# Kernel tuning notes

Hardware: AMD Instinct MI355X
Metric: run time of the kernel (lower is better)

## Reference

```python
import jax, jax.numpy as jnp
import numpy as np
from jax import lax


def _layernorm(x, scale, bias, eps=1e-5):
    m = x.mean(-1, keepdims=True)
    v = x.var(-1, keepdims=True)
    return (x - m) / jnp.sqrt(v + eps) * scale + bias


def setup_inputs() -> dict:
    key = jax.random.key(0)
    d = 21                      # code distance
    S = d * d - 1               # 440 tokens
    g = d + 1                   # 22x22 grid
    D, H, F, L, B = 256, 8, 512, 6, 64
    ks = jax.random.split(key, 24)
    w = 0.02
    idx = np.arange(S)
    scatter_positions = jnp.asarray(np.stack([idx // g, idx % g], axis=1), dtype=jnp.int64)
    inp = {
        'x': jax.random.randint(ks[0], (B, S), 0, 2).astype(jnp.int64),
        'scatter_positions': scatter_positions,
        'event_emb': w * jax.random.normal(ks[1], (2, D), jnp.float32),
        'pos_x': w * jax.random.normal(ks[2], (2 * d + 1, D), jnp.float32),
        'pos_y': w * jax.random.normal(ks[3], (2 * d + 1, D), jnp.float32),
        'stab_emb': w * jax.random.normal(ks[4], (2, D), jnp.float32),
        'tok_x': jax.random.randint(ks[5], (S,), 0, 2 * d + 1).astype(jnp.int64),
        'tok_y': jax.random.randint(ks[6], (S,), 0, 2 * d + 1).astype(jnp.int64),
        'tok_stab': jax.random.randint(ks[7], (S,), 0, 2).astype(jnp.int64),
        'attn_bias': w * jax.random.normal(ks[8], (S, S), jnp.float32),
        'Wqkv': w * jax.random.normal(ks[9], (L, 3 * D, D), jnp.float32),
        'bqkv': jnp.zeros((L, 3 * D), jnp.float32),
        'Wo': w * jax.random.normal(ks[10], (L, D, D), jnp.float32),
        'bo': jnp.zeros((L, D), jnp.float32),
        'W1': w * jax.random.normal(ks[11], (L, F, D), jnp.float32),
        'b1': jnp.zeros((L, F), jnp.float32),
        'W2': w * jax.random.normal(ks[12], (L, D, F), jnp.float32),
        'b2': jnp.zeros((L, D), jnp.float32),
        'ln1_s': jnp.ones((L, D), jnp.float32),
        'ln1_b': jnp.zeros((L, D), jnp.float32),
        'ln2_s': jnp.ones((L, D), jnp.float32),
        'ln2_b': jnp.zeros((L, D), jnp.float32),
        'cw1': w * jax.random.normal(ks[13], (L, D, D // H, 3, 3), jnp.float32),
        'cb1': jnp.zeros((L, D), jnp.float32),
        'cw2': w * jax.random.normal(ks[14], (L, D, D // H, 3, 3), jnp.float32),
        'cb2': jnp.zeros((L, D), jnp.float32),
        'cw3': w * jax.random.normal(ks[15], (L, D, D // H, 3, 3), jnp.float32),
        'cb3': jnp.zeros((L, D), jnp.float32),
    }
    return inp


def _forward(x, scatter_positions, event_emb, pos_x, pos_y, stab_emb, tok_x, tok_y,
             tok_stab, attn_bias, Wqkv, bqkv, Wo, bo, W1, b1, W2, b2,
             ln1_s, ln1_b, ln2_s, ln2_b, cw1, cb1, cw2, cb2, cw3, cb3):
    B, S = x.shape
    D = event_emb.shape[1]
    L = Wqkv.shape[0]
    H = D // cw1.shape[2]           # groups = n_heads
    dh = D // H
    g = int(np.sqrt(S + 1)) + 1     # (d+1) grid side
    rows = scatter_positions[:, 0]
    cols = scatter_positions[:, 1]

    # 2D positional encoding gathers + event embedding
    pos = pos_x[tok_x] + pos_y[tok_y] + stab_emb[tok_stab]   # [S, D]
    h = event_emb[x] + pos[None]                             # [B, S, D]

    scale = 1.0 / np.sqrt(dh).astype(np.float32)

    def conv(xg, wgt, b, dil):
        y = lax.conv_general_dilated(
            xg, wgt, window_strides=(1, 1), padding=[(dil, dil), (dil, dil)],
            rhs_dilation=(dil, dil), feature_group_count=H,
            dimension_numbers=('NCHW', 'OIHW', 'NCHW'))
        return jax.nn.relu(y + b[None, :, None, None])

    for l in range(L):
        # --- bias-MHA: QK^T * scale + learned relative bias, softmax, V ---
        qkv = jnp.einsum('bsd,ed->bse', h, Wqkv[l]) + bqkv[l]
        q, k, v = jnp.split(qkv, 3, axis=-1)
        q = q.reshape(B, S, H, dh)
        k = k.reshape(B, S, H, dh)
        v = v.reshape(B, S, H, dh)
        scores = jnp.einsum('bqhd,bkhd->bhqk', q, k) * scale + attn_bias[None, None]
        p = jax.nn.softmax(scores, axis=-1)
        o = jnp.einsum('bhqk,bkhd->bqhd', p, v).reshape(B, S, D)
        a = jnp.einsum('bsd,ed->bse', o, Wo[l]) + bo[l]
        h = _layernorm(h + a, ln1_s[l], ln1_b[l])
        # --- FFN (post-norm, ReLU) ---
        ff = jax.nn.relu(jnp.einsum('bsd,fd->bsf', h, W1[l]) + b1[l])
        ff = jnp.einsum('bsf,df->bsd', ff, W2[l]) + b2[l]
        h = _layernorm(h + ff, ln2_s[l], ln2_b[l])
        # --- scatter to 2D grid, grouped dilated convs, collect back ---
        grid = jnp.zeros((B, g, g, D), h.dtype).at[:, rows, cols].set(h)
        xg = grid.transpose(0, 3, 1, 2)                       # NCHW
        xg = 0.5 * (xg + conv(xg, cw1[l], cb1[l], 1)
                       + conv(xg, cw2[l], cb2[l], 2)
                       + conv(xg, cw3[l], cb3[l], 3))
        h = xg.transpose(0, 2, 3, 1)[:, rows, cols]           # collect_from_2d
    return h


def reference(x, scatter_positions, event_emb, pos_x, pos_y, stab_emb, tok_x, tok_y,
              tok_stab, attn_bias, Wqkv, bqkv, Wo, bo, W1, b1, W2, b2,
              ln1_s, ln1_b, ln2_s, ln2_b, cw1, cb1, cw2, cb2, cw3, cb3):
    return _forward(x, scatter_positions, event_emb, pos_x, pos_y, stab_emb, tok_x,
                    tok_y, tok_stab, attn_bias, Wqkv, bqkv, Wo, bo, W1, b1, W2, b2,
                    ln1_s, ln1_b, ln2_s, ln2_b, cw1, cb1, cw2, cb2, cw3, cb3)
```

## Files before the change

kernel.cpp:

```cpp
#include <hip/hip_runtime.h>
#include <hip/hip_bf16.h>

#define NB 64
#define S 440
#define D 256
#define H 8
#define DH 32
#define F 512
#define NL 6
#define G 22
#define NT (NB*S)
#define QBLK 224
#define QT2 2
#define PADK 456
#define CSTR 40

typedef __hip_bfloat16 bf16;
typedef unsigned short u16;
typedef __bf16 bf16x8 __attribute__((ext_vector_type(8)));
typedef float f32x4 __attribute__((ext_vector_type(4)));

#define MAGIC_BF16 0x3F803F80u

__device__ __align__(16) u16 g_abT[(S / 4) * S * 4];
#define WOFF_QKV 0
#define WOFF_WO  (NL*3*D*D)
#define WOFF_W1  (WOFF_WO + NL*D*D)
#define WOFF_W2  (WOFF_W1 + NL*F*D)
__device__ __align__(16) u16 g_wlin[WOFF_W2 + NL*D*F];
#define CVSTRIDE ((size_t)NL * 9 * 8 * 1024)
__device__ __align__(16) u16 g_cwt[3 * CVSTRIDE];
__device__ __align__(16) u16 g_qkvb[(size_t)NT * 768];
__device__ __align__(16) u16 g_obuf[(size_t)NT * D];
__device__ __align__(16) u16 g_acb [(size_t)NT * D];
__device__ __align__(16) u16 g_hbb [(size_t)NT * D];

static __device__ __forceinline__ float bf2f(bf16 x) { return __bfloat162float(x); }
static __device__ __forceinline__ float u2f(u16 u) {
  union { unsigned int i; float f; } t; t.i = ((unsigned int)u) << 16; return t.f;
}
static __device__ __forceinline__ float i2f(unsigned v) {
  union { unsigned u; float f; } t; t.u = v; return t.f;
}
static __device__ __forceinline__ u16 f2u(float f) {
  bf16 h = __float2bfloat16(f);
  return *(u16*)&h;
}
static __device__ __forceinline__ unsigned cvt_pk(float lo, float hi) {
  unsigned r;
  asm("v_cvt_pk_bf16_f32 %0, %1, %2" : "=v"(r) : "v"(lo), "v"(hi));
  return r;
}
static __device__ __forceinline__ float ldT(const void* p, size_t i, bool bfm) {
  return bfm ? u2f(((const u16*)p)[i]) : ((const float*)p)[i];
}
static __device__ __forceinline__ bf16x8 as_bf16x8(uint4 v) {
  union { uint4 u; bf16x8 b; } t; t.u = v; return t.b;
}
static __device__ __forceinline__ void gload_lds16(const u16* g, u16* l) {
  __builtin_amdgcn_global_load_lds(
      (const __attribute__((address_space(1))) void*)g,
      (__attribute__((address_space(3))) void*)l, 16, 0, 0);
}
static __device__ __forceinline__ const u16* selbuf(const void* ext, int sel) {
  return sel == 0 ? (const u16*)ext : sel == 1 ? g_hbb : sel == 2 ? g_qkvb : g_obuf;
}

__global__ void __launch_bounds__(256) cvt_conv(
    const void* __restrict__ src, int which, const unsigned* __restrict__ probe)
{
  bool bfm = (*probe == MAGIC_BF16);
  int n = NL * D * DH * 9;
  int i = blockIdx.x * 256 + threadIdx.x;
  if (i >= n) return;
  int kk = i % 9;
  int ic = (i / 9) % DH;
  int oc = (i / 288) % D;
  int l  = i / 73728;
  int g = oc >> 5, oc32 = oc & 31;
  u16 v;
  if (bfm) v = ((const u16*)src)[i];
  else     v = f2u(((const float*)src)[i]);
  g_cwt[(size_t)which * CVSTRIDE + (((size_t)l * 9 + kk) * 8 + g) * 1024 + oc32 * 32 + ic] = v;
}

__global__ void __launch_bounds__(256) cvt_lin(
    const void* __restrict__ src, size_t dstoff, int n,
    const unsigned* __restrict__ probe)
{
  bool bfm = (*probe == MAGIC_BF16);
  int i = blockIdx.x * 256 + threadIdx.x;
  if (i >= n) return;
  g_wlin[dstoff + i] = bfm ? ((const u16*)src)[i] : f2u(((const float*)src)[i]);
}

__global__ void __launch_bounds__(256) cvt_bias(
    const void* __restrict__ ab, const unsigned* __restrict__ probe)
{
  bool bfm = (*probe == MAGIC_BF16);
  int i = blockIdx.x * 256 + threadIdx.x;
  if (i >= (S / 4) * S * 4) return;
  int j = i & 3;
  int t = i >> 2;
  int q = t % S;
  int k4 = t / S;
  int k = k4 * 4 + j;
  float v = ldT(ab, (size_t)q * S + k, bfm) * 1.4426950408889634f;
  g_abT[i] = f2u(v);
}

__global__ void __launch_bounds__(256) embed_kernel(
    const int* __restrict__ x, const void* __restrict__ event_emb,
    const void* __restrict__ pos_x, const void* __restrict__ pos_y,
    const void* __restrict__ stab_emb, const int* __restrict__ tok_x,
    const int* __restrict__ tok_y, const int* __restrict__ tok_stab,
    bf16* __restrict__ h, const unsigned* __restrict__ probe)
{
  bool bfm = (*probe == MAGIC_BF16);
  int d = threadIdx.x;
#pragma unroll
  for (int r = 0; r < 4; ++r) {
    int t = blockIdx.x * 4 + r;
    int b = t / S, s = t - b * S;
    float v = ldT(event_emb, (size_t)x[b * S + s] * D + d, bfm)
            + ldT(pos_x, (size_t)tok_x[s] * D + d, bfm)
            + ldT(pos_y, (size_t)tok_y[s] * D + d, bfm)
            + ldT(stab_emb, (size_t)tok_stab[s] * D + d, bfm);
    h[(size_t)t * D + d] = __float2bfloat16(v);
  }
}

template <int RELU>
__global__ void __launch_bounds__(256) gemm_mfma(
    const void* __restrict__ Aext, int asel, size_t woff,
    const void* __restrict__ bias, size_t boff, int csel,
    int M, int N, int K, const unsigned* __restrict__ probe)
{
  bool bfm = (*probe == MAGIC_BF16);
  __shared__ u16 As[2][128][32];
  __shared__ u16 Ws[2][128][32];
  int tid = threadIdx.x;
  int bn = blockIdx.x, bm = blockIdx.y;
  int lane = tid & 63, w = tid >> 6;
  int wm = (w >> 1) * 64, wn = (w & 1) * 64;
  int qd = lane >> 4, ln16 = lane & 15;
  f32x4 zero4 = {0.f, 0.f, 0.f, 0.f};
  f32x4 acc[4][4];
#pragma unroll
  for (int i = 0; i < 4; ++i)
#pragma unroll
    for (int j = 0; j < 4; ++j) acc[i][j] = zero4;

  const u16* Au = selbuf(Aext, asel);
  u16* Cu = (csel == 0) ? g_qkvb : g_acb;
  const u16* Wu = g_wlin + woff;
  int srow = w * 32 + (lane >> 2);
  int skc  = (lane & 3) << 3;
  size_t abase = (size_t)(bm * 128 + srow) * K + skc;
  size_t wbase = (size_t)(bn * 128 + srow) * K + skc;

  gload_lds16(Au + abase,                   &As[0][w * 32][0]);
  gload_lds16(Au + abase + (size_t)16 * K,  &As[0][w * 32 + 16][0]);
  gload_lds16(Wu + wbase,                   &Ws[0][w * 32][0]);
  gload_lds16(Wu + wbase + (size_t)16 * K,  &Ws[0][w * 32 + 16][0]);

  int cur = 0;
  for (int k0 = 0; k0 < K; k0 += 32) {
    __syncthreads();
    if (k0 + 32 < K) {
      int nb = cur ^ 1;
      gload_lds16(Au + abase + k0 + 32,                  &As[nb][w * 32][0]);
      gload_lds16(Au + abase + (size_t)16 * K + k0 + 32, &As[nb][w * 32 + 16][0]);
      gload_lds16(Wu + wbase + k0 + 32,                  &Ws[nb][w * 32][0]);
      gload_lds16(Wu + wbase + (size_t)16 * K + k0 + 32, &Ws[nb][w * 32 + 16][0]);
    }
    bf16x8 af[4], bfr[4];
#pragma unroll
    for (int t = 0; t < 4; ++t) {
      af[t]  = *(const bf16x8*)&As[cur][wm + t * 16 + ln16][qd * 8];
      bfr[t] = *(const bf16x8*)&Ws[cur][wn + t * 16 + ln16][qd * 8];
    }
#pragma unroll
    for (int mt = 0; mt < 4; ++mt)
#pragma unroll
      for (int nt = 0; nt < 4; ++nt)
        acc[mt][nt] = __builtin_amdgcn_mfma_f32_16x16x32_bf16(af[mt], bfr[nt], acc[mt][nt], 0, 0, 0);
    cur ^= 1;
  }
#pragma unroll
  for (int nt = 0; nt < 4; ++nt) {
    int gcol = bn * 128 + wn + nt * 16 + ln16;
    float bv = ldT(bias, boff + gcol, bfm);
#pragma unroll
    for (int mt = 0; mt < 4; ++mt) {
#pragma unroll
      for (int r = 0; r < 4; ++r) {
        int grow = bm * 128 + wm + mt * 16 + qd * 4 + r;
        float v = acc[mt][nt][r] + bv;
        if (RELU) v = fmaxf(v, 0.f);
        Cu[(size_t)grow * N + gcol] = f2u(v);
      }
    }
  }
}

__global__ void __launch_bounds__(512) gemm_ln(
    const void* __restrict__ Aext, int asel, size_t woff,
    const void* __restrict__ bias, size_t boff,
    void* __restrict__ hext, int hsel,
    const void* __restrict__ sc, size_t soff,
    const void* __restrict__ bi, size_t boff2,
    int K, const unsigned* __restrict__ probe)
{
  bool bfm = (*probe == MAGIC_BF16);
  __shared__ u16 As[2][128][32];
  __shared__ u16 Ws[2][256][32];
  __shared__ float redS[4][128];
  __shared__ float redQ[4][128];
  int tid = threadIdx.x;
  int bm = blockIdx.x;
  int lane = tid & 63, w = tid >> 6;
  int wm = (w >> 2) * 64, wn = (w & 3) * 64;
  int qd = lane >> 4, ln16 = lane & 15;
  f32x4 zero4 = {0.f, 0.f, 0.f, 0.f};
  f32x4 acc[4][4];
#pragma unroll
  for (int i = 0; i < 4; ++i)
#pragma unroll
    for (int j = 0; j < 4; ++j) acc[i][j] = zero4;

  const u16* Au = selbuf(Aext, asel);
  u16* hp = hsel ? g_hbb : (u16*)hext;
  const u16* Wu = g_wlin + woff;
  int arow = w * 16 + (lane >> 2);
  int wrow = w * 32 + (lane >> 2);
  int skc  = (lane & 3) << 3;
  size_t abase = (size_t)(bm * 128 + arow) * K + skc;
  size_t wbase = (size_t)wrow * K + skc;

  gload_lds16(Au + abase,                  &As[0][w * 16][0]);
  gload_lds16(Wu + wbase,                  &Ws[0][w * 32][0]);
  gload_lds16(Wu + wbase + (size_t)16 * K, &Ws[0][w * 32 + 16][0]);

  int cur = 0;
  for (int k0 = 0; k0 < K; k0 += 32) {
    __syncthreads();
    if (k0 + 32 < K) {
      int nb = cur ^ 1;
      gload_lds16(Au + abase + k0 + 32,                  &As[nb][w * 16][0]);
      gload_lds16(Wu + wbase + k0 + 32,                  &Ws[nb][w * 32][0]);
      gload_lds16(Wu + wbase + (size_t)16 * K + k0 + 32, &Ws[nb][w * 32 + 16][0]);
    }
    bf16x8 af[4], bfr[4];
#pragma unroll
    for (int t = 0; t < 4; ++t) {
      af[t]  = *(const bf16x8*)&As[cur][wm + t * 16 + ln16][qd * 8];
      bfr[t] = *(const bf16x8*)&Ws[cur][wn + t * 16 + ln16][qd * 8];
    }
#pragma unroll
    for (int mt = 0; mt < 4; ++mt)
#pragma unroll
      for (int nt = 0; nt < 4; ++nt)
        acc[mt][nt] = __builtin_amdgcn_mfma_f32_16x16x32_bf16(af[mt], bfr[nt], acc[mt][nt], 0, 0, 0);
    cur ^= 1;
  }

  float bv[4];
#pragma unroll
  for (int nt = 0; nt < 4; ++nt) bv[nt] = ldT(bias, boff + wn + nt * 16 + ln16, bfm);
#pragma unroll
  for (int mt = 0; mt < 4; ++mt)
#pragma unroll
    for (int r = 0; r < 4; ++r) {
      size_t grow = (size_t)bm * 128 + wm + mt * 16 + qd * 4 + r;
#pragma unroll
      for (int nt = 0; nt < 4; ++nt) {
        int col = wn + nt * 16 + ln16;
        acc[mt][nt][r] += bv[nt] + u2f(hp[grow * D + col]);
      }
    }
#pragma unroll
  for (int mt = 0; mt < 4; ++mt)
#pragma unroll
    for (int r = 0; r < 4; ++r) {
      float s = (acc[mt][0][r] + acc[mt][1][r]) + (acc[mt][2][r] + acc[mt][3][r]);
      float q = (acc[mt][0][r] * acc[mt][0][r] + acc[mt][1][r] * acc[mt][1][r])
              + (acc[mt][2][r] * acc[mt][2][r] + acc[mt][3][r] * acc[mt][3][r]);
#pragma unroll
      for (int m = 1; m <= 8; m <<= 1) {
        s += __shfl_xor(s, m, 64);
        q += __shfl_xor(q, m, 64);
      }
      if (ln16 == 0) {
        int lrow = wm + mt * 16 + qd * 4 + r;
        redS[w & 3][lrow] = s;
        redQ[w & 3][lrow] = q;
      }
    }
  __syncthreads();
  float ls[4], lb[4];
#pragma unroll
  for (int nt = 0; nt < 4; ++nt) {
    ls[nt] = ldT(sc, soff + wn + nt * 16 + ln16, bfm);
    lb[nt] = ldT(bi, boff2 + wn + nt * 16 + ln16, bfm);
  }
#pragma unroll
  for (int mt = 0; mt < 4; ++mt)
#pragma unroll
    for (int r = 0; r < 4; ++r) {
      int lrow = wm + mt * 16 + qd * 4 + r;
      float Ssum = (redS[0][lrow] + redS[1][lrow]) + (redS[2][lrow] + redS[3][lrow]);
      float Qsum = (redQ[0][lrow] + redQ[1][lrow]) + (redQ[2][lrow] + redQ[3][lrow]);
      float mean = Ssum * (1.0f / D);
      float rstd = rsqrtf(Qsum * (1.0f / D) - mean * mean + 1e-5f);
      size_t grow = (size_t)bm * 128 + lrow;
#pragma unroll
      for (int nt = 0; nt < 4; ++nt) {
        int col = wn + nt * 16 + ln16;
        float o = (acc[mt][nt][r] - mean) * rstd * ls[nt] + lb[nt];
        hp[grow * D + col] = f2u(o);
      }
    }
}

__global__ void __launch_bounds__(448) attn_mfma()
{
  __shared__ u16 VT[32 * PADK];
  int tid = threadIdx.x;
  int blk = blockIdx.x;
  int qt = (blk >> 3) & 1;
  int bh = ((blk >> 4) << 3) | (blk & 7);
  int hh = bh % H;
  int b  = bh / H;
  int lane = tid & 63, w = tid >> 6;
  int qd = lane >> 4, ln16 = lane & 15;
  const u16* qkvu = g_qkvb;

  unsigned* VT32 = (unsigned*)VT;
#pragma unroll
  for (int i = 0; i < 2; ++i) {
    int slot = tid + i * 448;
    int rp = slot >> 2, kc = slot & 3;
    int r0 = rp * 2;
    uint4 va = make_uint4(0, 0, 0, 0), vb = make_uint4(0, 0, 0, 0);
    if (r0 < S)     va = *(const uint4*)&qkvu[((size_t)(b * S + r0)) * 768 + 512 + hh * DH + kc * 8];
    if (r0 + 1 < S) vb = *(const uint4*)&qkvu[((size_t)(b * S + r0 + 1)) * 768 + 512 + hh * DH + kc * 8];
    unsigned aw[4] = {va.x, va.y, va.z, va.w};
    unsigned bw[4] = {vb.x, vb.y, vb.z, vb.w};
#pragma unroll
    for (int jj = 0; jj < 4; ++jj) {
      int d = kc * 8 + jj * 2;
      VT32[(size_t)(d    ) * (PADK / 2) + rp] = (aw[jj] & 0xffffu) | ((bw[jj] & 0xffffu) << 16);
      VT32[(size_t)(d + 1) * (PADK / 2) + rp] = (aw[jj] >> 16)     | ((bw[jj] >> 16) << 16);
    }
  }

  int q0 = qt * QBLK + w * 32;
  int qaA = q0 + ln16;      if (qaA >= S) qaA = S - 1;
  int qaB = q0 + 16 + ln16; if (qaB >= S) qaB = S - 1;
  bf16x8 afA = *(const bf16x8*)&qkvu[((size_t)(b * S + qaA)) * 768 + hh * DH + qd * 8];
  bf16x8 afB = *(const bf16x8*)&qkvu[((size_t)(b * S + qaB)) * 768 + hh * DH + qd * 8];
  __syncthreads();

  int kperm = ((ln16 >> 2) << 3) + (ln16 & 3);
  auto kload = [&](int ks_, int half) -> uint4 {
    int tok = ks_ * 32 + kperm + half * 4;
    if (tok >= S) tok = S - 1;
    return *(const uint4*)&qkvu[((size_t)(b * S + tok)) * 768 + 256 + hh * DH + qd * 8];
  };
  uint4 kn0 = kload(0, 0), kn1 = kload(0, 1);

  float lsA = 0.f, lsB = 0.f;
  f32x4 zero4 = {0.f, 0.f, 0.f, 0.f};
  f32x4 oa0A = zero4, oa1A = zero4;
  f32x4 oa0B = zero4, oa1B = zero4;
  const float SC2 = 0.17677669529663689f * 1.4426950408889634f;

  auto bias4 = [&](uint2 wv, float* o) {
    o[0] = i2f(wv.x << 16); o[1] = i2f(wv.x & 0xffff0000u);
    o[2] = i2f(wv.y << 16); o[3] = i2f(wv.y & 0xffff0000u);
  };

  auto body = [&](int ks, bool masked) {
    int k4a = ks * 8 + 2 * qd;
    int k4b = k4a + 1;
    if (masked) { if (k4a > 109) k4a = 109; if (k4b > 109) k4b = 109; }
    uint2 bwaA = *(const uint2*)&g_abT[((size_t)k4a * S + qaA) * 4];
    uint2 bwbA = *(const uint2*)&g_abT[((size_t)k4b * S + qaA) * 4];
    uint2 bwaB = *(const uint2*)&g_abT[((size_t)k4a * S + qaB) * 4];
    uint2 bwbB = *(const uint2*)&g_abT[((size_t)k4b * S + qaB) * 4];
    bf16x8 kf0 = as_bf16x8(kn0), kf1 = as_bf16x8(kn1);
    if (!masked) { kn0 = kload(ks + 1, 0); kn1 = kload(ks + 1, 1); }
    f32x4 s0A = __builtin_amdgcn_mfma_f32_16x16x32_bf16(kf0, afA, zero4, 0, 0, 0);
    f32x4 s1A = __builtin_amdgcn_mfma_f32_16x16x32_bf16(kf1, afA, zero4, 0, 0, 0);
    f32x4 s0B = __builtin_amdgcn_mfma_f32_16x16x32_bf16(kf0, afB, zero4, 0, 0, 0);
    f32x4 s1B = __builtin_amdgcn_mfma_f32_16x16x32_bf16(kf1, afB, zero4, 0, 0, 0);
    float bAA[4], bBA[4], bAB[4], bBB[4];
    bias4(bwaA, bAA); bias4(bwbA, bBA); bias4(bwaB, bAB); bias4(bwbB, bBB);
    float pA[8], pB[8];
    if (!masked) {
#pragma unroll
      for (int r = 0; r < 4; ++r) {
        pA[r]     = exp2f(fminf(fmaf(s0A[r], SC2, bAA[r]), 80.f));
        pA[4 + r] = exp2f(fminf(fmaf(s1A[r], SC2, bBA[r]), 80.f));
        pB[r]     = exp2f(fminf(fmaf(s0B[r], SC2, bAB[r]), 80.f));
        pB[4 + r] = exp2f(fminf(fmaf(s1B[r], SC2, bBB[r]), 80.f));
      }
    } else {
      int c0 = ks * 32 + qd * 8;
#pragma unroll
      for (int r = 0; r < 4; ++r) {
        bool m0 = (c0 + r < S), m1 = (c0 + 4 + r < S);
        pA[r]     = exp2f(m0 ? fminf(fmaf(s0A[r], SC2, bAA[r]), 80.f) : -1e30f);
        pA[4 + r] = exp2f(m1 ? fminf(fmaf(s1A[r], SC2, bBA[r]), 80.f) : -1e30f);
        pB[r]     = exp2f(m0 ? fminf(fmaf(s0B[r], SC2, bAB[r]), 80.f) : -1e30f);
        pB[4 + r] = exp2f(m1 ? fminf(fmaf(s1B[r], SC2, bBB[r]), 80.f) : -1e30f);
      }
    }
    lsA += ((pA[0] + pA[1]) + (pA[2] + pA[3])) + ((pA[4] + pA[5]) + (pA[6] + pA[7]));
    lsB += ((pB[0] + pB[1]) + (pB[2] + pB[3])) + ((pB[4] + pB[5]) + (pB[6] + pB[7]));
    bf16x8 pfA = as_bf16x8(make_uint4(
        cvt_pk(pA[0], pA[1]), cvt_pk(pA[2], pA[3]),
        cvt_pk(pA[4], pA[5]), cvt_pk(pA[6], pA[7])));
    bf16x8 pfB = as_bf16x8(make_uint4(
        cvt_pk(pB[0], pB[1]), cvt_pk(pB[2], pB[3]),
        cvt_pk(pB[4], pB[5]), cvt_pk(pB[6], pB[7])));
    int kb = ks * 32;
    bf16x8 vf0 = *(const bf16x8*)&VT[(size_t)ln16 * PADK + kb + qd * 8];
    bf16x8 vf1 = *(const bf16x8*)&VT[(size_t)(16 + ln16) * PADK + kb + qd * 8];
    oa0A = __builtin_amdgcn_mfma_f32_16x16x32_bf16(vf0, pfA, oa0A, 0, 0, 0);
    oa1A = __builtin_amdgcn_mfma_f32_16x16x32_bf16(vf1, pfA, oa1A, 0, 0, 0);
    oa0B = __builtin_amdgcn_mfma_f32_16x16x32_bf16(vf0, pfB, oa0B, 0, 0, 0);
    oa1B = __builtin_amdgcn_mfma_f32_16x16x32_bf16(vf1, pfB, oa1B, 0, 0, 0);
  };

  for (int ks = 0; ks < 13; ++ks) body(ks, false);
  body(13, true);

  lsA += __shfl_xor(lsA, 16, 64);
  lsA += __shfl_xor(lsA, 32, 64);
  lsB += __shfl_xor(lsB, 16, 64);
  lsB += __shfl_xor(lsB, 32, 64);
  float invA = 1.0f / lsA, invB = 1.0f / lsB;
  int qA = q0 + ln16, qB = q0 + 16 + ln16;
  if (qA < S) {
    u16* op = g_obuf + ((size_t)(b * S + qA)) * D + hh * DH;
    *(uint2*)&op[qd * 4] = make_uint2(
        cvt_pk(oa0A[0] * invA, oa0A[1] * invA),
        cvt_pk(oa0A[2] * invA, oa0A[3] * invA));
    *(uint2*)&op[16 + qd * 4] = make_uint2(
        cvt_pk(oa1A[0] * invA, oa1A[1] * invA),
        cvt_pk(oa1A[2] * invA, oa1A[3] * invA));
  }
  if (qB < S) {
    u16* op = g_obuf + ((size_t)(b * S + qB)) * D + hh * DH;
    *(uint2*)&op[qd * 4] = make_uint2(
        cvt_pk(oa0B[0] * invB, oa0B[1] * invB),
        cvt_pk(oa0B[2] * invB, oa0B[3] * invB));
    *(uint2*)&op[16 + qd * 4] = make_uint2(
        cvt_pk(oa1B[0] * invB, oa1B[1] * invB),
        cvt_pk(oa1B[2] * invB, oa1B[3] * invB));
  }
}

__global__ void __launch_bounds__(256) conv_mfma(
    const void* __restrict__ hin_ext, int hinsel,
    const void* __restrict__ cb1, const void* __restrict__ cb2,
    const void* __restrict__ cb3, size_t cboff,
    void* __restrict__ hout_ext, int houtsel, int l, int final_,
    const unsigned* __restrict__ probe)
{
  bool bfm = (*probe == MAGIC_BF16);
  __shared__ u16 X[17 * 28 * CSTR];
  int half = blockIdx.x, g = blockIdx.y, b = blockIdx.z;
  int tid = threadIdx.x;
  int rb = half ? 7 : -3;
  const u16* hin = selbuf(hin_ext, hinsel);

  for (int i = tid; i < 17 * 28 * CSTR / 8; i += 256)
    *(uint4*)&X[i * 8] = make_uint4(0, 0, 0, 0);
  __syncthreads();
  int rv0 = half ? 7 : 0;
  int nrow = half ? 13 : 14;
  for (int i = tid; i < nrow * 22 * 4; i += 256) {
    int tk = i >> 2, ch = i & 3;
    int r = rv0 + tk / 22, c = tk % 22;
    uint4 v = *(const uint4*)&hin[((size_t)(b * S + r * 22 + c)) * D + g * 32 + ch * 8];
    *(uint4*)&X[(((r - rb) * 28) + (c + 3)) * CSTR + ch * 8] = v;
  }
  __syncthreads();

  int lane = tid & 63, w = tid >> 6;
  int qd = lane >> 4, ln16 = lane & 15;
  int nt = w & 1;
  int mq = w >> 1;
  int t_base = half * 224 + mq * 112;
  int oc_l = nt * 16 + ln16;

  int aoff[7];
#pragma unroll
  for (int mt = 0; mt < 7; ++mt) {
    int t = t_base + mt * 16 + ln16;
    if (t > S - 1) t = S - 1;
    int r = t / 22, c = t - r * 22;
    aoff[mt] = (((r - rb) * 28) + (c + 3)) * CSTR;
  }
  f32x4 fin[7];
#pragma unroll
  for (int mt = 0; mt < 7; ++mt) {
#pragma unroll
    for (int r4 = 0; r4 < 4; ++r4) {
      int t = t_base + mt * 16 + qd * 4 + r4;
      if (t > S - 1) t = S - 1;
      int r = t / 22, c = t - r * 22;
      fin[mt][r4] = u2f(X[(((r - rb) * 28) + (c + 3)) * CSTR + oc_l]);
    }
  }

  f32x4 zero4 = {0.f, 0.f, 0.f, 0.f};
  const void* cbs[3] = {cb1, cb2, cb3};
#pragma unroll
  for (int cv = 0; cv < 3; ++cv) {
    int dil = cv + 1;
    f32x4 acc[7];
#pragma unroll
    for (int mt = 0; mt < 7; ++mt) acc[mt] = zero4;
    const u16* wt = g_cwt + ((size_t)cv * NL + l) * (9 * 8 * 1024);
#pragma unroll
    for (int kk = 0; kk < 9; ++kk) {
      int off = ((kk / 3 - 1) * 28 + (kk % 3 - 1)) * dil * CSTR;
      bf16x8 bfrag = *(const bf16x8*)&wt[((size_t)kk * 8 + g) * 1024 + oc_l * 32 + qd * 8];
#pragma unroll
      for (int mt = 0; mt < 7; ++mt) {
        bf16x8 a = *(const bf16x8*)&X[aoff[mt] + off + qd * 8];
        acc[mt] = __builtin_amdgcn_mfma_f32_16x16x32_bf16(a, bfrag, acc[mt], 0, 0, 0);
      }
    }
    float bv = ldT(cbs[cv], cboff + g * 32 + oc_l, bfm);
#pragma unroll
    for (int mt = 0; mt < 7; ++mt)
#pragma unroll
      for (int r4 = 0; r4 < 4; ++r4)
        fin[mt][r4] += fmaxf(acc[mt][r4] + bv, 0.f);
  }

#pragma unroll
  for (int mt = 0; mt < 7; ++mt)
#pragma unroll
    for (int r4 = 0; r4 < 4; ++r4) {
      int t = t_base + mt * 16 + qd * 4 + r4;
      if (t < S) {
        float outv = 0.5f * fin[mt][r4];
        size_t oi = ((size_t)(b * S + t)) * D + g * 32 + oc_l;
        if (final_ && !bfm) ((float*)hout_ext)[oi] = outv;
        else {
          u16* ho = houtsel ? g_hbb : (u16*)hout_ext;
          ho[oi] = f2u(outv);
        }
      }
    }
}

extern "C" void kernel_launch(void* const* d_in, const int* in_sizes, int n_in,
                              void* d_out, int out_size, void* d_ws, size_t ws_size,
                              hipStream_t stream)
{
  const int*  x         = (const int*)d_in[0];
  const void* event_emb = d_in[2];
  const void* pos_x     = d_in[3];
  const void* pos_y     = d_in[4];
  const void* stab_emb  = d_in[5];
  const int*  tok_x     = (const int*)d_in[6];
  const int*  tok_y     = (const int*)d_in[7];
  const int*  tok_stab  = (const int*)d_in[8];
  const void* attn_bias = d_in[9];
  const void* Wqkv      = d_in[10];
  const void* bqkv      = d_in[11];
  const void* Wo        = d_in[12];
  const void* bo        = d_in[13];
  const void* W1        = d_in[14];
  const void* b1        = d_in[15];
  const void* W2        = d_in[16];
  const void* b2        = d_in[17];
  const void* ln1_s     = d_in[18];
  const void* ln1_b     = d_in[19];
  const void* ln2_s     = d_in[20];
  const void* ln2_b     = d_in[21];
  const void* cw1       = d_in[22];
  const void* cb1       = d_in[23];
  const void* cw2       = d_in[24];
  const void* cb2       = d_in[25];
  const void* cw3       = d_in[26];
  const void* cb3       = d_in[27];
  (void)in_sizes; (void)n_in; (void)out_size; (void)d_ws; (void)ws_size;
  const unsigned* probe = (const unsigned*)ln1_s;

  int ncv = NL * D * DH * 9;
  cvt_conv<<<(ncv + 255)/256, 256, 0, stream>>>(cw1, 0, probe);
  cvt_conv<<<(ncv + 255)/256, 256, 0, stream>>>(cw2, 1, probe);
  cvt_conv<<<(ncv + 255)/256, 256, 0, stream>>>(cw3, 2, probe);
  cvt_bias<<<((S/4)*S*4 + 255)/256, 256, 0, stream>>>(attn_bias, probe);
  cvt_lin<<<(NL*3*D*D + 255)/256, 256, 0, stream>>>(Wqkv, WOFF_QKV, NL*3*D*D, probe);
  cvt_lin<<<(NL*D*D   + 255)/256, 256, 0, stream>>>(Wo,   WOFF_WO,  NL*D*D,   probe);
  cvt_lin<<<(NL*F*D   + 255)/256, 256, 0, stream>>>(W1,   WOFF_W1,  NL*F*D,   probe);
  cvt_lin<<<(NL*D*F   + 255)/256, 256, 0, stream>>>(W2,   WOFF_W2,  NL*D*F,   probe);

  bf16* hout_ = (bf16*)d_out;
  embed_kernel<<<NT/4, 256, 0, stream>>>(x, event_emb, pos_x, pos_y, stab_emb,
                                         tok_x, tok_y, tok_stab, hout_, probe);

  for (int l = 0; l < NL; ++l) {
    int hs = l & 1;
    int fin = (l == NL - 1) ? 1 : 0;
    gemm_mfma<0><<<dim3(6, NT/128), 256, 0, stream>>>(
        hout_, hs, (size_t)WOFF_QKV + (size_t)l*3*D*D, bqkv, (size_t)l*3*D, 0,
        NT, 3*D, D, probe);
    attn_mfma<<<NB*H*QT2, 448, 0, stream>>>();
    gemm_ln<<<NT/128, 512, 0, stream>>>(
        hout_, 3, (size_t)WOFF_WO + (size_t)l*D*D, bo, (size_t)l*D,
        hout_, hs, ln1_s, (size_t)l*D, ln1_b, (size_t)l*D, D, probe);
    gemm_mfma<1><<<dim3(4, NT/128), 256, 0, stream>>>(
        hout_, hs, (size_t)WOFF_W1 + (size_t)l*F*D, b1, (size_t)l*F, 0,
        NT, F, D, probe);
    gemm_ln<<<NT/128, 512, 0, stream>>>(
        hout_, 2, (size_t)WOFF_W2 + (size_t)l*D*F, b2, (size_t)l*D,
        hout_, hs, ln2_s, (size_t)l*D, ln2_b, (size_t)l*D, F, probe);
    conv_mfma<<<dim3(2, 8, NB), 256, 0, stream>>>(
        hout_, hs, cb1, cb2, cb3, (size_t)l*D, hout_, hs ^ 1, l, fin, probe);
  }
}
```

Measured before the change: 1.264 ms.

## Process all queries of a head in one attention block, 64 per wave

The attention kernel no longer splits each (batch, head) across two query-tile blocks. Each wave now handles four 16-query fragments, so one block covers all 440 queries. This halves the redundant V-transpose staging into shared memory and the K fragment loads per query. The cost is higher register pressure, fewer blocks in the grid, and some wasted work on padded queries.

```diff
diff --git a/kernel.cpp b/kernel.cpp
--- a/kernel.cpp
+++ b/kernel.cpp
@@ -10,8 +10,6 @@
 #define NL 6
 #define G 22
 #define NT (NB*S)
-#define QBLK 224
-#define QT2 2
 #define PADK 456
 #define CSTR 40
 
@@ -327,9 +325,7 @@
 {
   __shared__ u16 VT[32 * PADK];
   int tid = threadIdx.x;
-  int blk = blockIdx.x;
-  int qt = (blk >> 3) & 1;
-  int bh = ((blk >> 4) << 3) | (blk & 7);
+  int bh = blockIdx.x;
   int hh = bh % H;
   int b  = bh / H;
   int lane = tid & 63, w = tid >> 6;
@@ -355,11 +351,15 @@
     }
   }
 
-  int q0 = qt * QBLK + w * 32;
-  int qaA = q0 + ln16;      if (qaA >= S) qaA = S - 1;
-  int qaB = q0 + 16 + ln16; if (qaB >= S) qaB = S - 1;
-  bf16x8 afA = *(const bf16x8*)&qkvu[((size_t)(b * S + qaA)) * 768 + hh * DH + qd * 8];
-  bf16x8 afB = *(const bf16x8*)&qkvu[((size_t)(b * S + qaB)) * 768 + hh * DH + qd * 8];
+  int q0 = w * 64;
+  int qa[4];
+  bf16x8 af[4];
+#pragma unroll
+  for (int f = 0; f < 4; ++f) {
+    int q = q0 + f * 16 + ln16; if (q >= S) q = S - 1;
+    qa[f] = q;
+    af[f] = *(const bf16x8*)&qkvu[((size_t)(b * S + q)) * 768 + hh * DH + qd * 8];
+  }
   __syncthreads();
 
   int kperm = ((ln16 >> 2) << 3) + (ln16 & 3);
@@ -370,96 +370,80 @@
   };
   uint4 kn0 = kload(0, 0), kn1 = kload(0, 1);
 
-  float lsA = 0.f, lsB = 0.f;
+  float lsum[4] = {0.f, 0.f, 0.f, 0.f};
   f32x4 zero4 = {0.f, 0.f, 0.f, 0.f};
-  f32x4 oa0A = zero4, oa1A = zero4;
-  f32x4 oa0B = zero4, oa1B = zero4;
+  f32x4 oa0[4], oa1[4];
+#pragma unroll
+  for (int f = 0; f < 4; ++f) { oa0[f] = zero4; oa1[f] = zero4; }
   const float SC2 = 0.17677669529663689f * 1.4426950408889634f;
-
-  auto bias4 = [&](uint2 wv, float* o) {
-    o[0] = i2f(wv.x << 16); o[1] = i2f(wv.x & 0xffff0000u);
-    o[2] = i2f(wv.y << 16); o[3] = i2f(wv.y & 0xffff0000u);
-  };
 
   auto body = [&](int ks, bool masked) {
     int k4a = ks * 8 + 2 * qd;
     int k4b = k4a + 1;
     if (masked) { if (k4a > 109) k4a = 109; if (k4b > 109) k4b = 109; }
-    uint2 bwaA = *(const uint2*)&g_abT[((size_t)k4a * S + qaA) * 4];
-    uint2 bwbA = *(const uint2*)&g_abT[((size_t)k4b * S + qaA) * 4];
-    uint2 bwaB = *(const uint2*)&g_abT[((size_t)k4a * S + qaB) * 4];
-    uint2 bwbB = *(const uint2*)&g_abT[((size_t)k4b * S + qaB) * 4];
+    uint2 bw0[4], bw1[4];
+#pragma unroll
+    for (int f = 0; f < 4; ++f) {
+      bw0[f] = *(const uint2*)&g_abT[((size_t)k4a * S + qa[f]) * 4];
+      bw1[f] = *(const uint2*)&g_abT[((size_t)k4b * S + qa[f]) * 4];
+    }
     bf16x8 kf0 = as_bf16x8(kn0), kf1 = as_bf16x8(kn1);
     if (!masked) { kn0 = kload(ks + 1, 0); kn1 = kload(ks + 1, 1); }
-    f32x4 s0A = __builtin_amdgcn_mfma_f32_16x16x32_bf16(kf0, afA, zero4, 0, 0, 0);
-    f32x4 s1A = __builtin_amdgcn_mfma_f32_16x16x32_bf16(kf1, afA, zero4, 0, 0, 0);
-    f32x4 s0B = __builtin_amdgcn_mfma_f32_16x16x32_bf16(kf0, afB, zero4, 0, 0, 0);
-    f32x4 s1B = __builtin_amdgcn_mfma_f32_16x16x32_bf16(kf1, afB, zero4, 0, 0, 0);
-    float bAA[4], bBA[4], bAB[4], bBB[4];
-    bias4(bwaA, bAA); bias4(bwbA, bBA); bias4(bwaB, bAB); bias4(bwbB, bBB);
-    float pA[8], pB[8];
-    if (!masked) {
-#pragma unroll
-      for (int r = 0; r < 4; ++r) {
-        pA[r]     = exp2f(fminf(fmaf(s0A[r], SC2, bAA[r]), 80.f));
-        pA[4 + r] = exp2f(fminf(fmaf(s1A[r], SC2, bBA[r]), 80.f));
-        pB[r]     = exp2f(fminf(fmaf(s0B[r], SC2, bAB[r]), 80.f));
-        pB[4 + r] = exp2f(fminf(fmaf(s1B[r], SC2, bBB[r]), 80.f));
-      }
-    } else {
-      int c0 = ks * 32 + qd * 8;
-#pragma unroll
-      for (int r = 0; r < 4; ++r) {
-        bool m0 = (c0 + r < S), m1 = (c0 + 4 + r < S);
-        pA[r]     = exp2f(m0 ? fminf(fmaf(s0A[r], SC2, bAA[r]), 80.f) : -1e30f);
-        pA[4 + r] = exp2f(m1 ? fminf(fmaf(s1A[r], SC2, bBA[r]), 80.f) : -1e30f);
-        pB[r]     = exp2f(m0 ? fminf(fmaf(s0B[r], SC2, bAB[r]), 80.f) : -1e30f);
-        pB[4 + r] = exp2f(m1 ? fminf(fmaf(s1B[r], SC2, bBB[r]), 80.f) : -1e30f);
-      }
-    }
-    lsA += ((pA[0] + pA[1]) + (pA[2] + pA[3])) + ((pA[4] + pA[5]) + (pA[6] + pA[7]));
-    lsB += ((pB[0] + pB[1]) + (pB[2] + pB[3])) + ((pB[4] + pB[5]) + (pB[6] + pB[7]));
-    bf16x8 pfA = as_bf16x8(make_uint4(
-        cvt_pk(pA[0], pA[1]), cvt_pk(pA[2], pA[3]),
-        cvt_pk(pA[4], pA[5]), cvt_pk(pA[6], pA[7])));
-    bf16x8 pfB = as_bf16x8(make_uint4(
-        cvt_pk(pB[0], pB[1]), cvt_pk(pB[2], pB[3]),
-        cvt_pk(pB[4], pB[5]), cvt_pk(pB[6], pB[7])));
     int kb = ks * 32;
     bf16x8 vf0 = *(const bf16x8*)&VT[(size_t)ln16 * PADK + kb + qd * 8];
     bf16x8 vf1 = *(const bf16x8*)&VT[(size_t)(16 + ln16) * PADK + kb + qd * 8];
-    oa0A = __builtin_amdgcn_mfma_f32_16x16x32_bf16(vf0, pfA, oa0A, 0, 0, 0);
-    oa1A = __builtin_amdgcn_mfma_f32_16x16x32_bf16(vf1, pfA, oa1A, 0, 0, 0);
-    oa0B = __builtin_amdgcn_mfma_f32_16x16x32_bf16(vf0, pfB, oa0B, 0, 0, 0);
-    oa1B = __builtin_amdgcn_mfma_f32_16x16x32_bf16(vf1, pfB, oa1B, 0, 0, 0);
+    int c0 = ks * 32 + qd * 8;
+#pragma unroll
+    for (int f = 0; f < 4; ++f) {
+      f32x4 s0 = __builtin_amdgcn_mfma_f32_16x16x32_bf16(kf0, af[f], zero4, 0, 0, 0);
+      f32x4 s1 = __builtin_amdgcn_mfma_f32_16x16x32_bf16(kf1, af[f], zero4, 0, 0, 0);
+      float bA[4] = { i2f(bw0[f].x << 16), i2f(bw0[f].x & 0xffff0000u),
+                      i2f(bw0[f].y << 16), i2f(bw0[f].y & 0xffff0000u) };
+      float bB[4] = { i2f(bw1[f].x << 16), i2f(bw1[f].x & 0xffff0000u),
+                      i2f(bw1[f].y << 16), i2f(bw1[f].y & 0xffff0000u) };
+      float p[8];
+      if (!masked) {
+#pragma unroll
+        for (int r = 0; r < 4; ++r) {
+          p[r]     = exp2f(fminf(fmaf(s0[r], SC2, bA[r]), 80.f));
+          p[4 + r] = exp2f(fminf(fmaf(s1[r], SC2, bB[r]), 80.f));
+        }
+      } else {
+#pragma unroll
+        for (int r = 0; r < 4; ++r) {
+          bool m0 = (c0 + r < S), m1 = (c0 + 4 + r < S);
+          p[r]     = exp2f(m0 ? fminf(fmaf(s0[r], SC2, bA[r]), 80.f) : -1e30f);
+          p[4 + r] = exp2f(m1 ? fminf(fmaf(s1[r], SC2, bB[r]), 80.f) : -1e30f);
+        }
+      }
+      lsum[f] += ((p[0] + p[1]) + (p[2] + p[3])) + ((p[4] + p[5]) + (p[6] + p[7]));
+      bf16x8 pf = as_bf16x8(make_uint4(
+          cvt_pk(p[0], p[1]), cvt_pk(p[2], p[3]),
+          cvt_pk(p[4], p[5]), cvt_pk(p[6], p[7])));
+      oa0[f] = __builtin_amdgcn_mfma_f32_16x16x32_bf16(vf0, pf, oa0[f], 0, 0, 0);
+      oa1[f] = __builtin_amdgcn_mfma_f32_16x16x32_bf16(vf1, pf, oa1[f], 0, 0, 0);
+    }
   };
 
   for (int ks = 0; ks < 13; ++ks) body(ks, false);
   body(13, true);
 
-  lsA += __shfl_xor(lsA, 16, 64);
-  lsA += __shfl_xor(lsA, 32, 64);
-  lsB += __shfl_xor(lsB, 16, 64);
-  lsB += __shfl_xor(lsB, 32, 64);
-  float invA = 1.0f / lsA, invB = 1.0f / lsB;
-  int qA = q0 + ln16, qB = q0 + 16 + ln16;
-  if (qA < S) {
-    u16* op = g_obuf + ((size_t)(b * S + qA)) * D + hh * DH;
-    *(uint2*)&op[qd * 4] = make_uint2(
-        cvt_pk(oa0A[0] * invA, oa0A[1] * invA),
-        cvt_pk(oa0A[2] * invA, oa0A[3] * invA));
-    *(uint2*)&op[16 + qd * 4] = make_uint2(
-        cvt_pk(oa1A[0] * invA, oa1A[1] * invA),
-        cvt_pk(oa1A[2] * invA, oa1A[3] * invA));
-  }
-  if (qB < S) {
-    u16* op = g_obuf + ((size_t)(b * S + qB)) * D + hh * DH;
-    *(uint2*)&op[qd * 4] = make_uint2(
-        cvt_pk(oa0B[0] * invB, oa0B[1] * invB),
-        cvt_pk(oa0B[2] * invB, oa0B[3] * invB));
-    *(uint2*)&op[16 + qd * 4] = make_uint2(
-        cvt_pk(oa1B[0] * invB, oa1B[1] * invB),
-        cvt_pk(oa1B[2] * invB, oa1B[3] * invB));
+#pragma unroll
+  for (int f = 0; f < 4; ++f) {
+    float l = lsum[f];
+    l += __shfl_xor(l, 16, 64);
+    l += __shfl_xor(l, 32, 64);
+    float inv = 1.0f / l;
+    int q = q0 + f * 16 + ln16;
+    if (q < S) {
+      u16* op = g_obuf + ((size_t)(b * S + q)) * D + hh * DH;
+      *(uint2*)&op[qd * 4] = make_uint2(
+          cvt_pk(oa0[f][0] * inv, oa0[f][1] * inv),
+          cvt_pk(oa0[f][2] * inv, oa0[f][3] * inv));
+      *(uint2*)&op[16 + qd * 4] = make_uint2(
+          cvt_pk(oa1[f][0] * inv, oa1[f][1] * inv),
+          cvt_pk(oa1[f][2] * inv, oa1[f][3] * inv));
+    }
   }
 }
 
@@ -615,7 +599,7 @@
     gemm_mfma<0><<<dim3(6, NT/128), 256, 0, stream>>>(
         hout_, hs, (size_t)WOFF_QKV + (size_t)l*3*D*D, bqkv, (size_t)l*3*D, 0,
         NT, 3*D, D, probe);
-    attn_mfma<<<NB*H*QT2, 448, 0, stream>>>();
+    attn_mfma<<<NB*H, 448, 0, stream>>>();
     gemm_ln<<<NT/128, 512, 0, stream>>>(
         hout_, 3, (size_t)WOFF_WO + (size_t)l*D*D, bo, (size_t)l*D,
         hout_, hs, ln1_s, (size_t)l*D, ln1_b, (size_t)l*D, D, probe);
```

New measurement: 1.270 ms. About the same (+0.5%).
